# Optimization experiments

Measured on AMD Instinct MI355X. Metric: run time of the kernel, lower is better.

Reference implementation:

```python
import jax, jax.numpy as jnp
import numpy as np

N_TRAIN = 16384
B_TEST = 4096
M_HALF = 768                 # modes per side -> M = 2*m+1 quadrature nodes
M_NODES = 2 * M_HALF + 1     # 1537
L_FFT = 4 * M_HALF + 1       # circulant embedding length (= 2*M-1)
H_SPACING = 0.01
SIGMASQ = 0.1
ELL = 0.1                    # SE kernel lengthscale
PROBES = 64
STEPS = 50
CG_ITERS = 50
TWO_PI = 2.0 * np.pi
EVAL_FLOOR = 1e-18


def setup_inputs():
    key = jax.random.key(0)
    k1, k2, k3, k4 = jax.random.split(key, 4)
    x = jax.random.uniform(k1, (N_TRAIN, 1), dtype=jnp.float32)
    y = jax.random.normal(k2, (N_TRAIN,), dtype=jnp.float32)
    x_new = jax.random.uniform(k3, (B_TEST, 1), dtype=jnp.float32)
    z = jax.random.normal(k4, (PROBES, M_NODES), dtype=jnp.float32)
    return {"x": x, "y": y, "x_new": x_new, "z": z}


def _cg(Aop, b, iters):
    """Conjugate gradients on Hermitian PD system, fixed iteration count."""
    x0 = jnp.zeros_like(b)
    rs0 = jnp.real(jnp.vdot(b, b))
    def step(carry, _):
        xk, rk, pk, rs = carry
        Ap = Aop(pk)
        a = (rs / jnp.real(jnp.vdot(pk, Ap))).astype(b.dtype)
        xk = xk + a * pk
        rk = rk - a * Ap
        rs_new = jnp.real(jnp.vdot(rk, rk))
        pk = rk + (rs_new / rs).astype(b.dtype) * pk
        return (xk, rk, pk, rs_new), None
    (xk, _, _, _), _ = jax.lax.scan(step, (x0, b, b, rs0), None, length=iters)
    return xk


def _efgp_forward(x, y, x_new, z):
    m = M_HALF
    ks = jnp.arange(-m, m + 1, dtype=jnp.float32)           # (M,)
    xis = H_SPACING * ks
    # squared-exponential spectral density, unit variance
    S = np.sqrt(TWO_PI) * ELL * jnp.exp(-2.0 * (np.pi * ELL * xis) ** 2)
    ws = jnp.sqrt(H_SPACING * S).astype(jnp.complex64)      # (M,) quadrature weights

    xf = x[:, 0]
    # convolution vector v[p] = sum_n exp(2*pi*i*h*p*x_n), p in [-2m, 2m]
    ps = jnp.arange(-2 * m, 2 * m + 1, dtype=jnp.float32)   # (L,)
    phase_v = (TWO_PI * H_SPACING) * jnp.outer(xf, ps)      # (N, L)
    vfull = jnp.exp(1j * phase_v).sum(axis=0)               # (L,) complex64
    # circulant first column c[q] = t[q] = v[-q]; T[j,k] = v[k-j]
    c = jnp.roll(vfull[::-1], 2 * m + 1)
    c_fft = jnp.fft.fft(c)

    def toeplitz(u):  # u: (..., M) complex -> (..., M)
        pad = jnp.zeros(u.shape[:-1] + (L_FFT - M_NODES,), u.dtype)
        upad = jnp.concatenate([u, pad], axis=-1)
        return jnp.fft.ifft(jnp.fft.fft(upad, axis=-1) * c_fft, axis=-1)[..., :M_NODES]

    # Fourier feature matrix F[n,k] = exp(2*pi*i*h*k*x_n)
    F = jnp.exp(1j * (TWO_PI * H_SPACING) * jnp.outer(xf, ks))  # (N, M)
    yc = y.astype(jnp.complex64)
    rhs = ws * (F.conj().T @ yc)                                 # ws * F^H y

    def A_mean(beta):  # ws T ws beta + sigma^2 beta
        return ws * toeplitz(ws * beta) + SIGMASQ * beta

    beta = _cg(A_mean, rhs, CG_ITERS)

    Fn = jnp.exp(1j * (TWO_PI * H_SPACING) * jnp.outer(x_new[:, 0], ks))  # (B, M)
    mean = jnp.real(Fn @ (ws * beta))                                      # (B,)

    # ---- stochastic Lanczos quadrature log-det of I + sigma^-2 D T D ----
    def Av(v):
        return v + (1.0 / SIGMASQ) * (ws * toeplitz(ws * v))

    zr = jnp.sign(z).astype(jnp.complex64)  # Rademacher probes (P, M)

    def lanczos(z1):
        nz2 = jnp.real(jnp.vdot(z1, z1))
        q0 = z1 / jnp.sqrt(nz2)
        def step(carry, _):
            q, q_prev, beta_prev = carry
            v = Av(q) - beta_prev * q_prev
            alpha = jnp.real(jnp.vdot(q, v))
            v = v - alpha * q
            beta = jnp.sqrt(jnp.real(jnp.vdot(v, v)))
            q_new = v / jnp.maximum(beta, 1e-12)
            return (q_new, q, beta), (alpha, beta)
        init = (q0, jnp.zeros_like(q0), jnp.zeros((), jnp.float32))
        _, (alphas, betas) = jax.lax.scan(step, init, None, length=STEPS)
        return alphas, betas, nz2

    alphas, betas, nz2 = jax.vmap(lanczos)(zr)  # (P, STEPS)

    def tridiag(a, b):
        return jnp.diag(a) + jnp.diag(b[:-1], 1) + jnp.diag(b[:-1], -1)

    Ts = jax.vmap(tridiag)(alphas, betas)       # (P, STEPS, STEPS)
    evals, evecs = jnp.linalg.eigh(Ts)
    evals = jnp.maximum(evals, EVAL_FLOOR)
    w1 = evecs[:, 0, :]                         # first component of each Ritz vector
    quad = jnp.sum(w1 ** 2 * jnp.log(evals), axis=-1) * nz2  # (P,)
    logdet = jnp.mean(quad) + N_TRAIN * np.log(SIGMASQ)

    alpha_vec = jnp.real(yc - F @ (ws * beta)) / SIGMASQ
    lml = -0.5 * jnp.dot(y, alpha_vec) - 0.5 * logdet \
          - 0.5 * N_TRAIN * np.log(2.0 * np.pi)
    return mean, lml


def reference(x, y, x_new, z):
    return _efgp_forward(x, y, x_new, z)
```

## Files before the change

kernel.cpp:

```cpp
#include <hip/hip_runtime.h>
#include <hip/hip_cooperative_groups.h>
#include <math.h>

namespace cg = cooperative_groups;

#define MN 1537
#define NFFT 4096
#define FBN (NFFT + NFFT/8)
#define CW 0.06283185307179587f
#define W4096 1.5339807878856412e-3f

__device__ __forceinline__ float2 cmulf(float2 a, float2 b) {
    return make_float2(a.x*b.x - a.y*b.y, a.x*b.y + a.y*b.x);
}
__device__ __forceinline__ float2 cadd(float2 a, float2 b){ return make_float2(a.x+b.x, a.y+b.y); }
__device__ __forceinline__ float2 csub(float2 a, float2 b){ return make_float2(a.x-b.x, a.y-b.y); }
__device__ __forceinline__ float2 mulnegi(float2 z){ return make_float2(z.y, -z.x); }
__device__ __forceinline__ float2 mulposi(float2 z){ return make_float2(-z.y, z.x); }
__device__ __forceinline__ float2 cconj(float2 z){ return make_float2(z.x, -z.y); }
__device__ __forceinline__ int PHI(int i){ return i + (i >> 3); }

__device__ __forceinline__ float ws_at(int k) {
    float xi = 0.01f * (float)(k - 768);
    float t  = 0.31415926535897931f * xi;
    float S  = 0.25066282746310002f * expf(-2.0f * t * t);
    return sqrtf(0.01f * S);
}

template<int S>
__device__ __forceinline__ void fwd8(float2* fb, int tt, float2 w1){
    const int Q = 1 << (S-2);
    const int p = tt & (Q-1);
    const int g = tt >> (S-2);
    const int base = (g << (S+1)) + p;
    float2 a0 = fb[PHI(base      )], a1 = fb[PHI(base +   Q)];
    float2 a2 = fb[PHI(base + 2*Q)], a3 = fb[PHI(base + 3*Q)];
    float2 a4 = fb[PHI(base + 4*Q)], a5 = fb[PHI(base + 5*Q)];
    float2 a6 = fb[PHI(base + 6*Q)], a7 = fb[PHI(base + 7*Q)];
    const float R = 0.70710678118654752f;
    float2 w2, w4, w1c1, w1c3;
    if (S == 2) {
        w1 = make_float2(1.f, 0.f); w2 = w1; w4 = w1;
        w1c1 = make_float2( R, -R); w1c3 = make_float2(-R, -R);
    } else {
        w2 = cmulf(w1, w1); w4 = cmulf(w2, w2);
        w1c1 = cmulf(w1, make_float2( R, -R));
        w1c3 = cmulf(w1, make_float2(-R, -R));
    }
    float2 b0 = cadd(a0,a4), b1 = cadd(a1,a5), b2 = cadd(a2,a6), b3 = cadd(a3,a7);
    float2 b4 = cmulf(csub(a0,a4), w1);
    float2 b5 = cmulf(csub(a1,a5), w1c1);
    float2 b6 = mulnegi(cmulf(csub(a2,a6), w1));
    float2 b7 = cmulf(csub(a3,a7), w1c3);
    float2 c0 = cadd(b0,b2), c2 = cmulf(csub(b0,b2), w2);
    float2 c1 = cadd(b1,b3), c3 = mulnegi(cmulf(csub(b1,b3), w2));
    float2 c4 = cadd(b4,b6), c6 = cmulf(csub(b4,b6), w2);
    float2 c5 = cadd(b5,b7), c7 = mulnegi(cmulf(csub(b5,b7), w2));
    fb[PHI(base      )] = cadd(c0,c1);
    fb[PHI(base +   Q)] = cmulf(csub(c0,c1), w4);
    fb[PHI(base + 2*Q)] = cadd(c2,c3);
    fb[PHI(base + 3*Q)] = cmulf(csub(c2,c3), w4);
    fb[PHI(base + 4*Q)] = cadd(c4,c5);
    fb[PHI(base + 5*Q)] = cmulf(csub(c4,c5), w4);
    fb[PHI(base + 6*Q)] = cadd(c6,c7);
    fb[PHI(base + 7*Q)] = cmulf(csub(c6,c7), w4);
}

template<int S>
__device__ __forceinline__ void inv8(float2* fb, int tt, float2 u1){
    const int Q = 1 << S;
    const int p = tt & (Q-1);
    const int g = tt >> S;
    const int base = (g << (S+3)) + p;
    float2 a0 = fb[PHI(base      )], a1 = fb[PHI(base +   Q)];
    float2 a2 = fb[PHI(base + 2*Q)], a3 = fb[PHI(base + 3*Q)];
    float2 a4 = fb[PHI(base + 4*Q)], a5 = fb[PHI(base + 5*Q)];
    float2 a6 = fb[PHI(base + 6*Q)], a7 = fb[PHI(base + 7*Q)];
    const float R = 0.70710678118654752f;
    float2 u2, u4, u1c1, u1c3;
    if (S == 0) {
        u1 = make_float2(1.f, 0.f); u2 = u1; u4 = u1;
        u1c1 = make_float2( R,  R); u1c3 = make_float2(-R,  R);
    } else {
        u2 = cmulf(u1, u1); u4 = cmulf(u2, u2);
        u1c1 = cmulf(u1, make_float2( R,  R));
        u1c3 = cmulf(u1, make_float2(-R,  R));
    }
    float2 m;
    m = cmulf(a1, u4); float2 t0 = cadd(a0,m), t1 = csub(a0,m);
    m = cmulf(a3, u4); float2 t2 = cadd(a2,m), t3 = csub(a2,m);
    m = cmulf(a5, u4); float2 t4 = cadd(a4,m), t5 = csub(a4,m);
    m = cmulf(a7, u4); float2 t6 = cadd(a6,m), t7 = csub(a6,m);
    m = cmulf(t2, u2);          float2 e0 = cadd(t0,m), e2 = csub(t0,m);
    m = mulposi(cmulf(t3, u2)); float2 e1 = cadd(t1,m), e3 = csub(t1,m);
    m = cmulf(t6, u2);          float2 e4 = cadd(t4,m), e6 = csub(t4,m);
    m = mulposi(cmulf(t7, u2)); float2 e5 = cadd(t5,m), e7 = csub(t5,m);
    m = cmulf(e4, u1);          fb[PHI(base      )] = cadd(e0,m); fb[PHI(base + 4*Q)] = csub(e0,m);
    m = cmulf(e5, u1c1);        fb[PHI(base +   Q)] = cadd(e1,m); fb[PHI(base + 5*Q)] = csub(e1,m);
    m = mulposi(cmulf(e6, u1)); fb[PHI(base + 2*Q)] = cadd(e2,m); fb[PHI(base + 6*Q)] = csub(e2,m);
    m = cmulf(e7, u1c3);        fb[PHI(base + 3*Q)] = cadd(e3,m); fb[PHI(base + 7*Q)] = csub(e3,m);
}

__device__ __forceinline__ void fwd8_first(float2* fb, int tt, float2 w1, const float2* in){
    const float R = 0.70710678118654752f;
    float2 w2 = cmulf(w1, w1), w4 = cmulf(w2, w2);
    float2 w1c1 = cmulf(w1, make_float2( R, -R));
    float2 w1c3 = cmulf(w1, make_float2(-R, -R));
    float2 b0 = in[0], b1 = in[1], b2 = in[2], b3 = in[3];
    float2 b4 = cmulf(in[0], w1);
    float2 b5 = cmulf(in[1], w1c1);
    float2 b6 = mulnegi(cmulf(in[2], w1));
    float2 b7 = cmulf(in[3], w1c3);
    float2 c0 = cadd(b0,b2), c2 = cmulf(csub(b0,b2), w2);
    float2 c1 = cadd(b1,b3), c3 = mulnegi(cmulf(csub(b1,b3), w2));
    float2 c4 = cadd(b4,b6), c6 = cmulf(csub(b4,b6), w2);
    float2 c5 = cadd(b5,b7), c7 = mulnegi(cmulf(csub(b5,b7), w2));
    fb[PHI(tt       )] = cadd(c0,c1);
    fb[PHI(tt +  512)] = cmulf(csub(c0,c1), w4);
    fb[PHI(tt + 1024)] = cadd(c2,c3);
    fb[PHI(tt + 1536)] = cmulf(csub(c2,c3), w4);
    fb[PHI(tt + 2048)] = cadd(c4,c5);
    fb[PHI(tt + 2560)] = cmulf(csub(c4,c5), w4);
    fb[PHI(tt + 3072)] = cadd(c6,c7);
    fb[PHI(tt + 3584)] = cmulf(csub(c6,c7), w4);
}

__device__ __forceinline__ void inv8_last(const float2* fb, int tt, float2 u1, float2* outv){
    const float R = 0.70710678118654752f;
    float2 u2 = cmulf(u1, u1), u4 = cmulf(u2, u2);
    float2 u1c1 = cmulf(u1, make_float2( R,  R));
    float2 u1c3 = cmulf(u1, make_float2(-R,  R));
    float2 a0 = fb[PHI(tt       )], a1 = fb[PHI(tt +  512)];
    float2 a2 = fb[PHI(tt + 1024)], a3 = fb[PHI(tt + 1536)];
    float2 a4 = fb[PHI(tt + 2048)], a5 = fb[PHI(tt + 2560)];
    float2 a6 = fb[PHI(tt + 3072)], a7 = fb[PHI(tt + 3584)];
    float2 m;
    m = cmulf(a1, u4); float2 t0 = cadd(a0,m), t1 = csub(a0,m);
    m = cmulf(a3, u4); float2 t2 = cadd(a2,m), t3 = csub(a2,m);
    m = cmulf(a5, u4); float2 t4 = cadd(a4,m), t5 = csub(a4,m);
    m = cmulf(a7, u4); float2 t6 = cadd(a6,m), t7 = csub(a6,m);
    m = cmulf(t2, u2);          float2 e0 = cadd(t0,m), e2 = csub(t0,m);
    m = mulposi(cmulf(t3, u2)); float2 e1 = cadd(t1,m), e3 = csub(t1,m);
    m = cmulf(t6, u2);          float2 e4 = cadd(t4,m), e6 = csub(t4,m);
    m = mulposi(cmulf(t7, u2)); float2 e5 = cadd(t5,m), e7 = csub(t5,m);
    outv[0] = cadd(e0, cmulf(e4, u1));
    outv[1] = cadd(e1, cmulf(e5, u1c1));
    outv[2] = cadd(e2, mulposi(cmulf(e6, u1)));
    outv[3] = cadd(e3, cmulf(e7, u1c3));
}

__device__ __forceinline__ void conv_fft(float2* fb, const float2* g, int tid,
                                         float2 t11, float2 t8, float2 t5,
                                         const float2* in, float2* outv){
    __syncthreads();
    fwd8_first(fb, tid, t11, in); __syncthreads();
    fwd8<8>(fb, tid, t8);  __syncthreads();
    fwd8<5>(fb, tid, t5);  __syncthreads();
    fwd8<2>(fb, tid, make_float2(1.f, 0.f)); __syncthreads();
    #pragma unroll
    for (int k = 0; k < 8; ++k){ int i = PHI(tid + k*512); fb[i] = cmulf(fb[i], g[k]); }
    __syncthreads();
    inv8<0>(fb, tid, make_float2(1.f, 0.f)); __syncthreads();
    inv8<3>(fb, tid, cconj(t5)); __syncthreads();
    inv8<6>(fb, tid, cconj(t8)); __syncthreads();
    inv8_last(fb, tid, cconj(t11), outv);
}

__device__ float block_reduce8(float v, volatile float* scratch) {
    int lane = threadIdx.x & 63;
    int wid  = threadIdx.x >> 6;
    #pragma unroll
    for (int off = 32; off > 0; off >>= 1) v += __shfl_down(v, off, 64);
    if (lane == 0) scratch[wid] = v;
    __syncthreads();
    if (wid == 0) {
        float s = (lane < 8) ? scratch[lane] : 0.0f;
        #pragma unroll
        for (int off = 4; off > 0; off >>= 1) s += __shfl_down(s, off, 64);
        if (lane == 0) scratch[16] = s;
    }
    __syncthreads();
    return scratch[16];
}

__global__ __launch_bounds__(512) __attribute__((amdgpu_waves_per_eu(2, 2)))
void mega(const float* __restrict__ x, const float* __restrict__ y,
          const float* __restrict__ xn, const float* __restrict__ z,
          float* __restrict__ out,
          float2* __restrict__ d_v, float2* __restrict__ d_rhs, float2* __restrict__ d_wb,
          float* __restrict__ d_al, float* __restrict__ d_be, float* __restrict__ d_nz2,
          float* __restrict__ d_quad, float* __restrict__ d_t1p)
{
    __shared__ float2 fb[FBN];
    __shared__ float  red[17];
    cg::grid_group grid = cg::this_grid();
    const int b = blockIdx.x, tid = threadIdx.x;
    const int wid = tid >> 6, lane = tid & 63;

    for (int c = b*8 + wid; c < 3073 + MN; c += 2048) {
        bool is_v = c < 3073;
        float pk = is_v ? (float)(c - 1536) : (float)(c - 3073 - 768);
        float sx = 0.f, sy = 0.f;
        if (is_v){
            for (int j = 0; j < 256; ++j){
                float ph = CW * (x[j*64 + lane] * pk);
                float s, cc; __sincosf(ph, &s, &cc);
                sx += cc; sy += s;
            }
        } else {
            for (int j = 0; j < 256; ++j){
                int n = j*64 + lane;
                float yv = y[n];
                float ph = CW * (x[n] * pk);
                float s, cc; __sincosf(ph, &s, &cc);
                sx += cc*yv; sy -= s*yv;
            }
        }
        #pragma unroll
        for (int off = 32; off > 0; off >>= 1){
            sx += __shfl_down(sx, off, 64);
            sy += __shfl_down(sy, off, 64);
        }
        if (lane == 0){
            if (is_v) d_v[c] = make_float2(sx, sy);
            else      d_rhs[c - 3073] = make_float2(sx, sy);
        }
    }
    grid.sync();

    if (b < 65) {
        float2 t11, t8, t5;
        { float a = -W4096 * (float)tid;               __sincosf(a, &t11.y, &t11.x); }
        { float a = -W4096 * (float)((tid & 63) << 3); __sincosf(a, &t8.y,  &t8.x ); }
        { float a = -W4096 * (float)((tid & 7)  << 6); __sincosf(a, &t5.y,  &t5.x ); }
        bool on3 = (tid == 0);
        float w[4];
        w[0] = ws_at(tid); w[1] = ws_at(tid + 512); w[2] = ws_at(tid + 1024);
        w[3] = on3 ? ws_at(1536) : 0.f;

        float2 g[8];
        #pragma unroll
        for (int k = 0; k < 8; ++k){
            int i = tid + k*512;
            float2 val = make_float2(0.f, 0.f);
            if (i == 0)            val = d_v[1536];
            else if (i <= 1536)    val = d_v[1536 - i];
            else if (i >= 2560)    val = d_v[5632 - i];
            fb[PHI(i)] = val;
        }
        __syncthreads();
        fwd8<11>(fb, tid, t11); __syncthreads();
        fwd8<8 >(fb, tid, t8);  __syncthreads();
        fwd8<5 >(fb, tid, t5);  __syncthreads();
        fwd8<2 >(fb, tid, make_float2(1.f, 0.f)); __syncthreads();
        #pragma unroll
        for (int k = 0; k < 8; ++k) g[k] = fb[PHI(tid + k*512)];

        float2 sin_[4], cv[4];
        if (b < 64) {
            float2 q[4], qp[4];
            float part = 0.f;
            #pragma unroll
            for (int s = 0; s < 4; ++s){
                float sv = 0.f;
                if (s < 3 || on3){
                    float zv = z[b*MN + tid + s*512];
                    sv = (zv > 0.f) ? 1.f : ((zv < 0.f) ? -1.f : 0.f);
                }
                q[s] = make_float2(sv, 0.f);
                qp[s] = make_float2(0.f, 0.f);
                part += sv * sv;
            }
            float nz2 = block_reduce8(part, red);
            if (tid == 0) d_nz2[b] = nz2;
            float qs = 1.0f / sqrtf(nz2);
            #pragma unroll
            for (int s = 0; s < 4; ++s){ q[s].x *= qs; q[s].y *= qs; }
            float bp = 0.f;
            float cf[4];
            #pragma unroll
            for (int s = 0; s < 4; ++s) cf[s] = w[s] * (10.0f / 4096.0f);
            for (int step = 0; step < 50; ++step) {
                #pragma unroll
                for (int s = 0; s < 4; ++s)
                    sin_[s] = make_float2(w[s]*q[s].x, w[s]*q[s].y);
                conv_fft(fb, g, tid, t11, t8, t5, sin_, cv);
                float2 v[4];
                part = 0.f;
                #pragma unroll
                for (int s = 0; s < 4; ++s){
                    v[s] = make_float2(q[s].x + cf[s]*cv[s].x - bp*qp[s].x,
                                       q[s].y + cf[s]*cv[s].y - bp*qp[s].y);
                    part += q[s].x*v[s].x + q[s].y*v[s].y;
                }
                float alpha = block_reduce8(part, red);
                part = 0.f;
                #pragma unroll
                for (int s = 0; s < 4; ++s){
                    v[s].x -= alpha*q[s].x; v[s].y -= alpha*q[s].y;
                    part += v[s].x*v[s].x + v[s].y*v[s].y;
                }
                float nv = block_reduce8(part, red);
                float beta = sqrtf(nv);
                if (tid == 0) { d_al[b*50 + step] = alpha; d_be[b*50 + step] = beta; }
                float binv = 1.0f / fmaxf(beta, 1e-12f);
                #pragma unroll
                for (int s = 0; s < 4; ++s){
                    qp[s] = q[s];
                    q[s] = make_float2(v[s].x*binv, v[s].y*binv);
                }
                bp = beta;
            }
        } else {
            float2 r[4], p[4], xx[4];
            float part = 0.f;
            #pragma unroll
            for (int s = 0; s < 4; ++s){
                float2 bj = make_float2(0.f, 0.f);
                if (s < 3 || on3){
                    float2 rr = d_rhs[tid + s*512];
                    bj = make_float2(w[s]*rr.x, w[s]*rr.y);
                }
                r[s] = bj; p[s] = bj; xx[s] = make_float2(0.f, 0.f);
                part += bj.x*bj.x + bj.y*bj.y;
            }
            float rs = block_reduce8(part, red);
            float cf[4];
            #pragma unroll
            for (int s = 0; s < 4; ++s) cf[s] = w[s] * (1.0f / 4096.0f);
            for (int it = 0; it < 50; ++it) {
                #pragma unroll
                for (int s = 0; s < 4; ++s)
                    sin_[s] = make_float2(w[s]*p[s].x, w[s]*p[s].y);
                conv_fft(fb, g, tid, t11, t8, t5, sin_, cv);
                float2 ap[4];
                part = 0.f;
                #pragma unroll
                for (int s = 0; s < 4; ++s){
                    ap[s] = make_float2(cf[s]*cv[s].x + 0.1f*p[s].x,
                                        cf[s]*cv[s].y + 0.1f*p[s].y);
                    part += p[s].x*ap[s].x + p[s].y*ap[s].y;
                }
                float pAp = block_reduce8(part, red);
                float a = rs / pAp;
                part = 0.f;
                #pragma unroll
                for (int s = 0; s < 4; ++s){
                    xx[s].x += a*p[s].x; xx[s].y += a*p[s].y;
                    r[s].x -= a*ap[s].x; r[s].y -= a*ap[s].y;
                    part += r[s].x*r[s].x + r[s].y*r[s].y;
                }
                float rsn = block_reduce8(part, red);
                float sc = rsn / rs;
                #pragma unroll
                for (int s = 0; s < 4; ++s)
                    p[s] = make_float2(r[s].x + sc*p[s].x, r[s].y + sc*p[s].y);
                rs = rsn;
            }
            #pragma unroll
            for (int s = 0; s < 4; ++s){
                if (s < 3 || on3)
                    d_wb[tid + s*512] = make_float2(w[s]*xx[s].x, w[s]*xx[s].y);
            }
        }
    }
    grid.sync();

    if (b < 64) {
        if (tid < 64) {
            float* sa  = (float*)fb;
            float* se  = sa + 64;
            float* se2 = sa + 128;
            int t = tid;
            if (t < 50) {
                sa[t] = d_al[b*50 + t];
                float bv = (t < 49) ? d_be[b*50 + t] : 0.0f;
                se[t] = bv; se2[t] = bv * bv;
            }
            float quad = 0.0f;
            if (t < 50) {
                float lo = 3.4e38f, hi = -3.4e38f;
                for (int i = 0; i < 50; ++i) {
                    float rr = ((i > 0) ? fabsf(se[i-1]) : 0.0f) + ((i < 49) ? fabsf(se[i]) : 0.0f);
                    lo = fminf(lo, sa[i] - rr);
                    hi = fmaxf(hi, sa[i] + rr);
                }
                for (int it = 0; it < 38; ++it) {
                    float mid = 0.5f * (lo + hi);
                    int cnt = 0;
                    float qq = sa[0] - mid;
                    cnt += (qq < 0.0f);
                    for (int k = 1; k < 50; ++k) {
                        float dnm = (fabsf(qq) < 1e-30f) ? ((qq < 0.0f) ? -1e-30f : 1e-30f) : qq;
                        qq = (sa[k] - mid) - se2[k-1] * __builtin_amdgcn_rcpf(dnm);
                        cnt += (qq < 0.0f);
                    }
                    if (cnt > t) hi = mid; else lo = mid;
                }
                float lam = 0.5f * (lo + hi);
                float pm = 0.0f, pc = 1.0f, s = 1.0f, bprev = 0.0f;
                for (int k = 0; k < 49; ++k) {
                    float bk = fmaxf(se[k], 1e-30f);
                    float pn = ((lam - sa[k]) * pc - bprev * pm) * __builtin_amdgcn_rcpf(bk);
                    pn = fminf(fmaxf(pn, -1e18f), 1e18f);
                    s += pn * pn;
                    pm = pc; pc = pn; bprev = bk;
                }
                quad = logf(fmaxf(lam, 1e-18f)) / s;
            }
            #pragma unroll
            for (int off = 32; off > 0; off >>= 1) quad += __shfl_down(quad, off, 64);
            if (t == 0) d_quad[b] = quad * d_nz2[b];
        }
    } else if (b < 96) {
        int row = (b - 64)*128 + (tid >> 2);
        int sub = tid & 3;
        float xv = xn[row];
        float acc = 0.f;
        for (int k = sub; k < MN; k += 4) {
            float ph = CW * (xv * (float)(k - 768));
            float s, c; __sincosf(ph, &s, &c);
            float2 ww = d_wb[k];
            acc += c * ww.x - s * ww.y;
        }
        acc += __shfl_down(acc, 2, 4);
        acc += __shfl_down(acc, 1, 4);
        if (sub == 0) out[row] = acc;
    } else if (b < 224) {
        int n = (b - 96)*128 + (tid >> 2);
        int sub = tid & 3;
        float xv = x[n], yv = y[n];
        float acc = 0.f;
        for (int k = sub; k < MN; k += 4) {
            float ph = CW * (xv * (float)(k - 768));
            float s, c; __sincosf(ph, &s, &c);
            float2 ww = d_wb[k];
            acc += c * ww.x - s * ww.y;
        }
        acc += __shfl_down(acc, 2, 4);
        acc += __shfl_down(acc, 1, 4);
        float contrib = (sub == 0) ? yv * (yv - acc) * 10.0f : 0.f;
        #pragma unroll
        for (int off = 32; off > 0; off >>= 1) contrib += __shfl_down(contrib, off, 64);
        if (lane == 0) red[wid] = contrib;
        __syncthreads();
        if (tid == 0) {
            float s = 0.f;
            #pragma unroll
            for (int i = 0; i < 8; ++i) s += red[i];
            d_t1p[b - 96] = s;
        }
    }
    grid.sync();

    if (b == 0 && tid < 64) {
        float qv = d_quad[tid];
        float t1 = d_t1p[tid] + d_t1p[tid + 64];
        #pragma unroll
        for (int off = 32; off > 0; off >>= 1) {
            qv += __shfl_down(qv, off, 64);
            t1 += __shfl_down(t1, off, 64);
        }
        if (tid == 0) {
            float ld = qv / 64.0f - 37725.5542f;
            out[4096] = -0.5f * t1 - 0.5f * ld - 15055.8889f;
        }
    }
}

extern "C" void kernel_launch(void* const* d_in, const int* in_sizes, int n_in,
                              void* d_out, int out_size, void* d_ws, size_t ws_size,
                              hipStream_t stream) {
    const float* d_x  = (const float*)d_in[0];
    const float* d_y  = (const float*)d_in[1];
    const float* d_xn = (const float*)d_in[2];
    const float* d_z  = (const float*)d_in[3];
    float* out = (float*)d_out;
    char* w = (char*)d_ws;
    float2* d_v   = (float2*)(w + 0);
    float2* d_rhs = (float2*)(w + 24832);
    float2* d_wb  = (float2*)(w + 37376);
    float*  d_al  = (float*)(w + 49920);
    float*  d_be  = (float*)(w + 62720);
    float*  d_nz2 = (float*)(w + 75520);
    float*  d_quad= (float*)(w + 75776);
    float*  d_t1p = (float*)(w + 76032);

    void* args[] = { (void*)&d_x, (void*)&d_y, (void*)&d_xn, (void*)&d_z, (void*)&out,
                     (void*)&d_v, (void*)&d_rhs, (void*)&d_wb, (void*)&d_al, (void*)&d_be,
                     (void*)&d_nz2, (void*)&d_quad, (void*)&d_t1p };
    hipLaunchCooperativeKernel((const void*)mega, dim3(256), dim3(512), args, 0, stream);
}
```

Baseline: 513.3 us.

## Fuse FFT middle stages with spectral multiply, merge Lanczos reductions, precompute twiddles

```diff
diff --git a/kernel.cpp b/kernel.cpp
--- a/kernel.cpp
+++ b/kernel.cpp
@@ -6,7 +6,7 @@
 
 #define MN 1537
 #define NFFT 4096
-#define FBN (NFFT + NFFT/8)
+#define FBN (NFFT + NFFT/8 + NFFT/64)
 #define CW 0.06283185307179587f
 #define W4096 1.5339807878856412e-3f
 
@@ -18,7 +18,7 @@
 __device__ __forceinline__ float2 mulnegi(float2 z){ return make_float2(z.y, -z.x); }
 __device__ __forceinline__ float2 mulposi(float2 z){ return make_float2(-z.y, z.x); }
 __device__ __forceinline__ float2 cconj(float2 z){ return make_float2(z.x, -z.y); }
-__device__ __forceinline__ int PHI(int i){ return i + (i >> 3); }
+__device__ __forceinline__ int PHI(int i){ return i + (i >> 3) + (i >> 6); }
 
 __device__ __forceinline__ float ws_at(int k) {
     float xi = 0.01f * (float)(k - 768);
@@ -27,8 +27,21 @@
     return sqrtf(0.01f * S);
 }
 
+struct Tw { float2 w1, w2, w4, c1, c3; };
+
+__device__ __forceinline__ Tw make_tw(float ang){
+    Tw t;
+    __sincosf(ang, &t.w1.y, &t.w1.x);
+    t.w2 = cmulf(t.w1, t.w1);
+    t.w4 = cmulf(t.w2, t.w2);
+    const float R = 0.70710678118654752f;
+    t.c1 = cmulf(t.w1, make_float2( R, -R));
+    t.c3 = cmulf(t.w1, make_float2(-R, -R));
+    return t;
+}
+
 template<int S>
-__device__ __forceinline__ void fwd8(float2* fb, int tt, float2 w1){
+__device__ __forceinline__ void fwd8c(float2* fb, int tt, const Tw& w){
     const int Q = 1 << (S-2);
     const int p = tt & (Q-1);
     const int g = tt >> (S-2);
@@ -37,55 +50,37 @@
     float2 a2 = fb[PHI(base + 2*Q)], a3 = fb[PHI(base + 3*Q)];
     float2 a4 = fb[PHI(base + 4*Q)], a5 = fb[PHI(base + 5*Q)];
     float2 a6 = fb[PHI(base + 6*Q)], a7 = fb[PHI(base + 7*Q)];
-    const float R = 0.70710678118654752f;
-    float2 w2, w4, w1c1, w1c3;
-    if (S == 2) {
-        w1 = make_float2(1.f, 0.f); w2 = w1; w4 = w1;
-        w1c1 = make_float2( R, -R); w1c3 = make_float2(-R, -R);
-    } else {
-        w2 = cmulf(w1, w1); w4 = cmulf(w2, w2);
-        w1c1 = cmulf(w1, make_float2( R, -R));
-        w1c3 = cmulf(w1, make_float2(-R, -R));
-    }
     float2 b0 = cadd(a0,a4), b1 = cadd(a1,a5), b2 = cadd(a2,a6), b3 = cadd(a3,a7);
-    float2 b4 = cmulf(csub(a0,a4), w1);
-    float2 b5 = cmulf(csub(a1,a5), w1c1);
-    float2 b6 = mulnegi(cmulf(csub(a2,a6), w1));
-    float2 b7 = cmulf(csub(a3,a7), w1c3);
-    float2 c0 = cadd(b0,b2), c2 = cmulf(csub(b0,b2), w2);
-    float2 c1 = cadd(b1,b3), c3 = mulnegi(cmulf(csub(b1,b3), w2));
-    float2 c4 = cadd(b4,b6), c6 = cmulf(csub(b4,b6), w2);
-    float2 c5 = cadd(b5,b7), c7 = mulnegi(cmulf(csub(b5,b7), w2));
+    float2 b4 = cmulf(csub(a0,a4), w.w1);
+    float2 b5 = cmulf(csub(a1,a5), w.c1);
+    float2 b6 = mulnegi(cmulf(csub(a2,a6), w.w1));
+    float2 b7 = cmulf(csub(a3,a7), w.c3);
+    float2 c0 = cadd(b0,b2), c2 = cmulf(csub(b0,b2), w.w2);
+    float2 c1 = cadd(b1,b3), c3 = mulnegi(cmulf(csub(b1,b3), w.w2));
+    float2 c4 = cadd(b4,b6), c6 = cmulf(csub(b4,b6), w.w2);
+    float2 c5 = cadd(b5,b7), c7 = mulnegi(cmulf(csub(b5,b7), w.w2));
     fb[PHI(base      )] = cadd(c0,c1);
-    fb[PHI(base +   Q)] = cmulf(csub(c0,c1), w4);
+    fb[PHI(base +   Q)] = cmulf(csub(c0,c1), w.w4);
     fb[PHI(base + 2*Q)] = cadd(c2,c3);
-    fb[PHI(base + 3*Q)] = cmulf(csub(c2,c3), w4);
+    fb[PHI(base + 3*Q)] = cmulf(csub(c2,c3), w.w4);
     fb[PHI(base + 4*Q)] = cadd(c4,c5);
-    fb[PHI(base + 5*Q)] = cmulf(csub(c4,c5), w4);
+    fb[PHI(base + 5*Q)] = cmulf(csub(c4,c5), w.w4);
     fb[PHI(base + 6*Q)] = cadd(c6,c7);
-    fb[PHI(base + 7*Q)] = cmulf(csub(c6,c7), w4);
+    fb[PHI(base + 7*Q)] = cmulf(csub(c6,c7), w.w4);
 }
 
 template<int S>
-__device__ __forceinline__ void inv8(float2* fb, int tt, float2 u1){
+__device__ __forceinline__ void inv8c(float2* fb, int tt, const Tw& w){
     const int Q = 1 << S;
     const int p = tt & (Q-1);
     const int g = tt >> S;
     const int base = (g << (S+3)) + p;
+    float2 u1 = cconj(w.w1), u2 = cconj(w.w2), u4 = cconj(w.w4);
+    float2 uc1 = cconj(w.c1), uc3 = cconj(w.c3);
     float2 a0 = fb[PHI(base      )], a1 = fb[PHI(base +   Q)];
     float2 a2 = fb[PHI(base + 2*Q)], a3 = fb[PHI(base + 3*Q)];
     float2 a4 = fb[PHI(base + 4*Q)], a5 = fb[PHI(base + 5*Q)];
     float2 a6 = fb[PHI(base + 6*Q)], a7 = fb[PHI(base + 7*Q)];
-    const float R = 0.70710678118654752f;
-    float2 u2, u4, u1c1, u1c3;
-    if (S == 0) {
-        u1 = make_float2(1.f, 0.f); u2 = u1; u4 = u1;
-        u1c1 = make_float2( R,  R); u1c3 = make_float2(-R,  R);
-    } else {
-        u2 = cmulf(u1, u1); u4 = cmulf(u2, u2);
-        u1c1 = cmulf(u1, make_float2( R,  R));
-        u1c3 = cmulf(u1, make_float2(-R,  R));
-    }
     float2 m;
     m = cmulf(a1, u4); float2 t0 = cadd(a0,m), t1 = csub(a0,m);
     m = cmulf(a3, u4); float2 t2 = cadd(a2,m), t3 = csub(a2,m);
@@ -96,40 +91,34 @@
     m = cmulf(t6, u2);          float2 e4 = cadd(t4,m), e6 = csub(t4,m);
     m = mulposi(cmulf(t7, u2)); float2 e5 = cadd(t5,m), e7 = csub(t5,m);
     m = cmulf(e4, u1);          fb[PHI(base      )] = cadd(e0,m); fb[PHI(base + 4*Q)] = csub(e0,m);
-    m = cmulf(e5, u1c1);        fb[PHI(base +   Q)] = cadd(e1,m); fb[PHI(base + 5*Q)] = csub(e1,m);
+    m = cmulf(e5, uc1);         fb[PHI(base +   Q)] = cadd(e1,m); fb[PHI(base + 5*Q)] = csub(e1,m);
     m = mulposi(cmulf(e6, u1)); fb[PHI(base + 2*Q)] = cadd(e2,m); fb[PHI(base + 6*Q)] = csub(e2,m);
-    m = cmulf(e7, u1c3);        fb[PHI(base + 3*Q)] = cadd(e3,m); fb[PHI(base + 7*Q)] = csub(e3,m);
-}
-
-__device__ __forceinline__ void fwd8_first(float2* fb, int tt, float2 w1, const float2* in){
-    const float R = 0.70710678118654752f;
-    float2 w2 = cmulf(w1, w1), w4 = cmulf(w2, w2);
-    float2 w1c1 = cmulf(w1, make_float2( R, -R));
-    float2 w1c3 = cmulf(w1, make_float2(-R, -R));
+    m = cmulf(e7, uc3);         fb[PHI(base + 3*Q)] = cadd(e3,m); fb[PHI(base + 7*Q)] = csub(e3,m);
+}
+
+__device__ __forceinline__ void fwd8_first(float2* fb, int tt, const Tw& w, const float2* in){
     float2 b0 = in[0], b1 = in[1], b2 = in[2], b3 = in[3];
-    float2 b4 = cmulf(in[0], w1);
-    float2 b5 = cmulf(in[1], w1c1);
-    float2 b6 = mulnegi(cmulf(in[2], w1));
-    float2 b7 = cmulf(in[3], w1c3);
-    float2 c0 = cadd(b0,b2), c2 = cmulf(csub(b0,b2), w2);
-    float2 c1 = cadd(b1,b3), c3 = mulnegi(cmulf(csub(b1,b3), w2));
-    float2 c4 = cadd(b4,b6), c6 = cmulf(csub(b4,b6), w2);
-    float2 c5 = cadd(b5,b7), c7 = mulnegi(cmulf(csub(b5,b7), w2));
+    float2 b4 = cmulf(in[0], w.w1);
+    float2 b5 = cmulf(in[1], w.c1);
+    float2 b6 = mulnegi(cmulf(in[2], w.w1));
+    float2 b7 = cmulf(in[3], w.c3);
+    float2 c0 = cadd(b0,b2), c2 = cmulf(csub(b0,b2), w.w2);
+    float2 c1 = cadd(b1,b3), c3 = mulnegi(cmulf(csub(b1,b3), w.w2));
+    float2 c4 = cadd(b4,b6), c6 = cmulf(csub(b4,b6), w.w2);
+    float2 c5 = cadd(b5,b7), c7 = mulnegi(cmulf(csub(b5,b7), w.w2));
     fb[PHI(tt       )] = cadd(c0,c1);
-    fb[PHI(tt +  512)] = cmulf(csub(c0,c1), w4);
+    fb[PHI(tt +  512)] = cmulf(csub(c0,c1), w.w4);
     fb[PHI(tt + 1024)] = cadd(c2,c3);
-    fb[PHI(tt + 1536)] = cmulf(csub(c2,c3), w4);
+    fb[PHI(tt + 1536)] = cmulf(csub(c2,c3), w.w4);
     fb[PHI(tt + 2048)] = cadd(c4,c5);
-    fb[PHI(tt + 2560)] = cmulf(csub(c4,c5), w4);
+    fb[PHI(tt + 2560)] = cmulf(csub(c4,c5), w.w4);
     fb[PHI(tt + 3072)] = cadd(c6,c7);
-    fb[PHI(tt + 3584)] = cmulf(csub(c6,c7), w4);
-}
-
-__device__ __forceinline__ void inv8_last(const float2* fb, int tt, float2 u1, float2* outv){
-    const float R = 0.70710678118654752f;
-    float2 u2 = cmulf(u1, u1), u4 = cmulf(u2, u2);
-    float2 u1c1 = cmulf(u1, make_float2( R,  R));
-    float2 u1c3 = cmulf(u1, make_float2(-R,  R));
+    fb[PHI(tt + 3584)] = cmulf(csub(c6,c7), w.w4);
+}
+
+__device__ __forceinline__ void inv8_last(const float2* fb, int tt, const Tw& w, float2* outv){
+    float2 u1 = cconj(w.w1), u2 = cconj(w.w2), u4 = cconj(w.w4);
+    float2 uc1 = cconj(w.c1), uc3 = cconj(w.c3);
     float2 a0 = fb[PHI(tt       )], a1 = fb[PHI(tt +  512)];
     float2 a2 = fb[PHI(tt + 1024)], a3 = fb[PHI(tt + 1536)];
     float2 a4 = fb[PHI(tt + 2048)], a5 = fb[PHI(tt + 2560)];
@@ -144,43 +133,120 @@
     m = cmulf(t6, u2);          float2 e4 = cadd(t4,m), e6 = csub(t4,m);
     m = mulposi(cmulf(t7, u2)); float2 e5 = cadd(t5,m), e7 = csub(t5,m);
     outv[0] = cadd(e0, cmulf(e4, u1));
-    outv[1] = cadd(e1, cmulf(e5, u1c1));
+    outv[1] = cadd(e1, cmulf(e5, uc1));
     outv[2] = cadd(e2, mulposi(cmulf(e6, u1)));
-    outv[3] = cadd(e3, cmulf(e7, u1c3));
+    outv[3] = cadd(e3, cmulf(e7, uc3));
+}
+
+__device__ __forceinline__ void mid8(float2* fb, int tt, const float2* g){
+    const float R = 0.70710678118654752f;
+    const int base = tt << 3;
+    float2 a0 = fb[PHI(base  )], a1 = fb[PHI(base+1)];
+    float2 a2 = fb[PHI(base+2)], a3 = fb[PHI(base+3)];
+    float2 a4 = fb[PHI(base+4)], a5 = fb[PHI(base+5)];
+    float2 a6 = fb[PHI(base+6)], a7 = fb[PHI(base+7)];
+    float2 b0 = cadd(a0,a4), b1 = cadd(a1,a5), b2 = cadd(a2,a6), b3 = cadd(a3,a7);
+    float2 b4 = csub(a0,a4);
+    float2 b5 = cmulf(csub(a1,a5), make_float2( R, -R));
+    float2 b6 = mulnegi(csub(a2,a6));
+    float2 b7 = cmulf(csub(a3,a7), make_float2(-R, -R));
+    float2 c0 = cadd(b0,b2), c2 = csub(b0,b2);
+    float2 c1 = cadd(b1,b3), c3 = mulnegi(csub(b1,b3));
+    float2 c4 = cadd(b4,b6), c6 = csub(b4,b6);
+    float2 c5 = cadd(b5,b7), c7 = mulnegi(csub(b5,b7));
+    float2 d0 = cadd(c0,c1), d1 = csub(c0,c1);
+    float2 d2 = cadd(c2,c3), d3 = csub(c2,c3);
+    float2 d4 = cadd(c4,c5), d5 = csub(c4,c5);
+    float2 d6 = cadd(c6,c7), d7 = csub(c6,c7);
+    d0 = cmulf(d0, g[0]); d1 = cmulf(d1, g[1]); d2 = cmulf(d2, g[2]); d3 = cmulf(d3, g[3]);
+    d4 = cmulf(d4, g[4]); d5 = cmulf(d5, g[5]); d6 = cmulf(d6, g[6]); d7 = cmulf(d7, g[7]);
+    float2 m;
+    m = d1; float2 t0 = cadd(d0,m), t1 = csub(d0,m);
+    m = d3; float2 t2 = cadd(d2,m), t3 = csub(d2,m);
+    m = d5; float2 t4 = cadd(d4,m), t5 = csub(d4,m);
+    m = d7; float2 t6 = cadd(d6,m), t7 = csub(d6,m);
+    m = t2;          float2 e0 = cadd(t0,m), e2 = csub(t0,m);
+    m = mulposi(t3); float2 e1 = cadd(t1,m), e3 = csub(t1,m);
+    m = t6;          float2 e4 = cadd(t4,m), e6 = csub(t4,m);
+    m = mulposi(t7); float2 e5 = cadd(t5,m), e7 = csub(t5,m);
+    m = e4;                           fb[PHI(base  )] = cadd(e0,m); fb[PHI(base+4)] = csub(e0,m);
+    m = cmulf(e5, make_float2(R, R)); fb[PHI(base+1)] = cadd(e1,m); fb[PHI(base+5)] = csub(e1,m);
+    m = mulposi(e6);                  fb[PHI(base+2)] = cadd(e2,m); fb[PHI(base+6)] = csub(e2,m);
+    m = cmulf(e7, make_float2(-R, R));fb[PHI(base+3)] = cadd(e3,m); fb[PHI(base+7)] = csub(e3,m);
+}
+
+__device__ __forceinline__ void fwd8_last_reg(const float2* fb, int tt, float2* gout){
+    const float R = 0.70710678118654752f;
+    const int base = tt << 3;
+    float2 a0 = fb[PHI(base  )], a1 = fb[PHI(base+1)];
+    float2 a2 = fb[PHI(base+2)], a3 = fb[PHI(base+3)];
+    float2 a4 = fb[PHI(base+4)], a5 = fb[PHI(base+5)];
+    float2 a6 = fb[PHI(base+6)], a7 = fb[PHI(base+7)];
+    float2 b0 = cadd(a0,a4), b1 = cadd(a1,a5), b2 = cadd(a2,a6), b3 = cadd(a3,a7);
+    float2 b4 = csub(a0,a4);
+    float2 b5 = cmulf(csub(a1,a5), make_float2( R, -R));
+    float2 b6 = mulnegi(csub(a2,a6));
+    float2 b7 = cmulf(csub(a3,a7), make_float2(-R, -R));
+    float2 c0 = cadd(b0,b2), c2 = csub(b0,b2);
+    float2 c1 = cadd(b1,b3), c3 = mulnegi(csub(b1,b3));
+    float2 c4 = cadd(b4,b6), c6 = csub(b4,b6);
+    float2 c5 = cadd(b5,b7), c7 = mulnegi(csub(b5,b7));
+    gout[0] = cadd(c0,c1); gout[1] = csub(c0,c1);
+    gout[2] = cadd(c2,c3); gout[3] = csub(c2,c3);
+    gout[4] = cadd(c4,c5); gout[5] = csub(c4,c5);
+    gout[6] = cadd(c6,c7); gout[7] = csub(c6,c7);
 }
 
 __device__ __forceinline__ void conv_fft(float2* fb, const float2* g, int tid,
-                                         float2 t11, float2 t8, float2 t5,
+                                         const Tw& T11, const Tw& T8, const Tw& T5,
                                          const float2* in, float2* outv){
     __syncthreads();
-    fwd8_first(fb, tid, t11, in); __syncthreads();
-    fwd8<8>(fb, tid, t8);  __syncthreads();
-    fwd8<5>(fb, tid, t5);  __syncthreads();
-    fwd8<2>(fb, tid, make_float2(1.f, 0.f)); __syncthreads();
-    #pragma unroll
-    for (int k = 0; k < 8; ++k){ int i = PHI(tid + k*512); fb[i] = cmulf(fb[i], g[k]); }
-    __syncthreads();
-    inv8<0>(fb, tid, make_float2(1.f, 0.f)); __syncthreads();
-    inv8<3>(fb, tid, cconj(t5)); __syncthreads();
-    inv8<6>(fb, tid, cconj(t8)); __syncthreads();
-    inv8_last(fb, tid, cconj(t11), outv);
-}
-
-__device__ float block_reduce8(float v, volatile float* scratch) {
-    int lane = threadIdx.x & 63;
-    int wid  = threadIdx.x >> 6;
+    fwd8_first(fb, tid, T11, in); __syncthreads();
+    fwd8c<8>(fb, tid, T8); __syncthreads();
+    fwd8c<5>(fb, tid, T5); __syncthreads();
+    mid8(fb, tid, g);      __syncthreads();
+    inv8c<3>(fb, tid, T5); __syncthreads();
+    inv8c<6>(fb, tid, T8); __syncthreads();
+    inv8_last(fb, tid, T11, outv);
+}
+
+__device__ float block_reduce8(float v, volatile float* sc) {
+    int lane = threadIdx.x & 63, wid = threadIdx.x >> 6;
     #pragma unroll
     for (int off = 32; off > 0; off >>= 1) v += __shfl_down(v, off, 64);
-    if (lane == 0) scratch[wid] = v;
+    if (lane == 0) sc[wid] = v;
     __syncthreads();
     if (wid == 0) {
-        float s = (lane < 8) ? scratch[lane] : 0.0f;
+        float s = (lane < 8) ? sc[lane] : 0.0f;
         #pragma unroll
         for (int off = 4; off > 0; off >>= 1) s += __shfl_down(s, off, 64);
-        if (lane == 0) scratch[16] = s;
+        if (lane == 0) sc[16] = s;
     }
     __syncthreads();
-    return scratch[16];
+    return sc[16];
+}
+
+__device__ float2 block_reduce2(float2 v, volatile float* sc) {
+    int lane = threadIdx.x & 63, wid = threadIdx.x >> 6;
+    #pragma unroll
+    for (int off = 32; off > 0; off >>= 1) {
+        v.x += __shfl_down(v.x, off, 64);
+        v.y += __shfl_down(v.y, off, 64);
+    }
+    if (lane == 0) { sc[wid] = v.x; sc[17 + wid] = v.y; }
+    __syncthreads();
+    if (wid == 0) {
+        float sx = (lane < 8) ? sc[lane] : 0.0f;
+        float sy = (lane < 8) ? sc[17 + lane] : 0.0f;
+        #pragma unroll
+        for (int off = 4; off > 0; off >>= 1) {
+            sx += __shfl_down(sx, off, 64);
+            sy += __shfl_down(sy, off, 64);
+        }
+        if (lane == 0) { sc[16] = sx; sc[33] = sy; }
+    }
+    __syncthreads();
+    return make_float2(sc[16], sc[33]);
 }
 
 __global__ __launch_bounds__(512) __attribute__((amdgpu_waves_per_eu(2, 2)))
@@ -192,7 +258,7 @@
           float* __restrict__ d_quad, float* __restrict__ d_t1p)
 {
     __shared__ float2 fb[FBN];
-    __shared__ float  red[17];
+    __shared__ float  redb[40];
     cg::grid_group grid = cg::this_grid();
     const int b = blockIdx.x, tid = threadIdx.x;
     const int wid = tid >> 6, lane = tid & 63;
@@ -229,10 +295,9 @@
     grid.sync();
 
     if (b < 65) {
-        float2 t11, t8, t5;
-        { float a = -W4096 * (float)tid;               __sincosf(a, &t11.y, &t11.x); }
-        { float a = -W4096 * (float)((tid & 63) << 3); __sincosf(a, &t8.y,  &t8.x ); }
-        { float a = -W4096 * (float)((tid & 7)  << 6); __sincosf(a, &t5.y,  &t5.x ); }
+        Tw T11 = make_tw(-W4096 * (float)tid);
+        Tw T8  = make_tw(-W4096 * (float)((tid & 63) << 3));
+        Tw T5  = make_tw(-W4096 * (float)((tid & 7)  << 6));
         bool on3 = (tid == 0);
         float w[4];
         w[0] = ws_at(tid); w[1] = ws_at(tid + 512); w[2] = ws_at(tid + 1024);
@@ -249,12 +314,10 @@
             fb[PHI(i)] = val;
         }
         __syncthreads();
-        fwd8<11>(fb, tid, t11); __syncthreads();
-        fwd8<8 >(fb, tid, t8);  __syncthreads();
-        fwd8<5 >(fb, tid, t5);  __syncthreads();
-        fwd8<2 >(fb, tid, make_float2(1.f, 0.f)); __syncthreads();
-        #pragma unroll
-        for (int k = 0; k < 8; ++k) g[k] = fb[PHI(tid + k*512)];
+        fwd8c<11>(fb, tid, T11); __syncthreads();
+        fwd8c<8 >(fb, tid, T8);  __syncthreads();
+        fwd8c<5 >(fb, tid, T5);  __syncthreads();
+        fwd8_last_reg(fb, tid, g);
 
         float2 sin_[4], cv[4];
         if (b < 64) {
@@ -271,7 +334,7 @@
                 qp[s] = make_float2(0.f, 0.f);
                 part += sv * sv;
             }
-            float nz2 = block_reduce8(part, red);
+            float nz2 = block_reduce8(part, redb);
             if (tid == 0) d_nz2[b] = nz2;
             float qs = 1.0f / sqrtf(nz2);
             #pragma unroll
@@ -284,30 +347,27 @@
                 #pragma unroll
                 for (int s = 0; s < 4; ++s)
                     sin_[s] = make_float2(w[s]*q[s].x, w[s]*q[s].y);
-                conv_fft(fb, g, tid, t11, t8, t5, sin_, cv);
+                conv_fft(fb, g, tid, T11, T8, T5, sin_, cv);
                 float2 v[4];
-                part = 0.f;
+                float2 pp = make_float2(0.f, 0.f);
                 #pragma unroll
                 for (int s = 0; s < 4; ++s){
                     v[s] = make_float2(q[s].x + cf[s]*cv[s].x - bp*qp[s].x,
                                        q[s].y + cf[s]*cv[s].y - bp*qp[s].y);
-                    part += q[s].x*v[s].x + q[s].y*v[s].y;
-                }
-                float alpha = block_reduce8(part, red);
-                part = 0.f;
-                #pragma unroll
-                for (int s = 0; s < 4; ++s){
-                    v[s].x -= alpha*q[s].x; v[s].y -= alpha*q[s].y;
-                    part += v[s].x*v[s].x + v[s].y*v[s].y;
-                }
-                float nv = block_reduce8(part, red);
-                float beta = sqrtf(nv);
+                    pp.x += q[s].x*v[s].x + q[s].y*v[s].y;
+                    pp.y += v[s].x*v[s].x + v[s].y*v[s].y;
+                }
+                float2 rr = block_reduce2(pp, redb);
+                float alpha = rr.x;
+                float beta = sqrtf(fmaxf(rr.y - alpha*alpha, 0.f));
                 if (tid == 0) { d_al[b*50 + step] = alpha; d_be[b*50 + step] = beta; }
                 float binv = 1.0f / fmaxf(beta, 1e-12f);
                 #pragma unroll
                 for (int s = 0; s < 4; ++s){
+                    float2 nq = make_float2((v[s].x - alpha*q[s].x)*binv,
+                                            (v[s].y - alpha*q[s].y)*binv);
                     qp[s] = q[s];
-                    q[s] = make_float2(v[s].x*binv, v[s].y*binv);
+                    q[s] = nq;
                 }
                 bp = beta;
             }
@@ -318,13 +378,13 @@
             for (int s = 0; s < 4; ++s){
                 float2 bj = make_float2(0.f, 0.f);
                 if (s < 3 || on3){
-                    float2 rr = d_rhs[tid + s*512];
-                    bj = make_float2(w[s]*rr.x, w[s]*rr.y);
+                    float2 rv = d_rhs[tid + s*512];
+                    bj = make_float2(w[s]*rv.x, w[s]*rv.y);
                 }
                 r[s] = bj; p[s] = bj; xx[s] = make_float2(0.f, 0.f);
                 part += bj.x*bj.x + bj.y*bj.y;
             }
-            float rs = block_reduce8(part, red);
+            float rs = block_reduce8(part, redb);
             float cf[4];
             #pragma unroll
             for (int s = 0; s < 4; ++s) cf[s] = w[s] * (1.0f / 4096.0f);
@@ -332,7 +392,7 @@
                 #pragma unroll
                 for (int s = 0; s < 4; ++s)
                     sin_[s] = make_float2(w[s]*p[s].x, w[s]*p[s].y);
-                conv_fft(fb, g, tid, t11, t8, t5, sin_, cv);
+                conv_fft(fb, g, tid, T11, T8, T5, sin_, cv);
                 float2 ap[4];
                 part = 0.f;
                 #pragma unroll
@@ -341,7 +401,7 @@
                                         cf[s]*cv[s].y + 0.1f*p[s].y);
                     part += p[s].x*ap[s].x + p[s].y*ap[s].y;
                 }
-                float pAp = block_reduce8(part, red);
+                float pAp = block_reduce8(part, redb);
                 float a = rs / pAp;
                 part = 0.f;
                 #pragma unroll
@@ -350,7 +410,7 @@
                     r[s].x -= a*ap[s].x; r[s].y -= a*ap[s].y;
                     part += r[s].x*r[s].x + r[s].y*r[s].y;
                 }
-                float rsn = block_reduce8(part, red);
+                float rsn = block_reduce8(part, redb);
                 float sc = rsn / rs;
                 #pragma unroll
                 for (int s = 0; s < 4; ++s)
@@ -442,12 +502,12 @@
         float contrib = (sub == 0) ? yv * (yv - acc) * 10.0f : 0.f;
         #pragma unroll
         for (int off = 32; off > 0; off >>= 1) contrib += __shfl_down(contrib, off, 64);
-        if (lane == 0) red[wid] = contrib;
+        if (lane == 0) redb[wid] = contrib;
         __syncthreads();
         if (tid == 0) {
             float s = 0.f;
             #pragma unroll
-            for (int i = 0; i < 8; ++i) s += red[i];
+            for (int i = 0; i < 8; ++i) s += redb[i];
             d_t1p[b - 96] = s;
         }
     }
```

Measured after the change: 477.6 us. 1.07x faster.
